# Performance work log

Measured on AMD Instinct MI355X. Metric: run time of the kernel, lower is better.

The kernel has to match this reference:

```python
import jax, jax.numpy as jnp
import numpy as np

B, IN, C, H, E = 8192, 768, 64, 64, 16  # batch, input_dim, n_concepts, hidden_dim, embedding_dim


def setup_inputs() -> dict:
    key = jax.random.key(0)
    ks = jax.random.split(key, 10)

    def w(k, shape, fan_in):
        return jax.random.normal(k, shape, jnp.float32) / np.float32(np.sqrt(fan_in))

    inp = {"x": jax.random.normal(ks[0], (B, IN), jnp.float32)}
    i = 1
    for pre, din, dout in (("pos", IN, E), ("neg", IN, E), ("cp", 2 * E, 1)):
        inp[pre + "_W1"] = w(ks[i], (C, din, H), din)
        inp[pre + "_b1"] = jnp.zeros((C, H), jnp.float32)
        inp[pre + "_W2"] = w(ks[i + 1], (C, H, H), H)
        inp[pre + "_b2"] = jnp.zeros((C, H), jnp.float32)
        inp[pre + "_W3"] = w(ks[i + 2], (C, H, dout), H)
        inp[pre + "_b3"] = jnp.zeros((C, dout), jnp.float32)
        i += 3
    return inp


def _bank(x, W1, b1, W2, b2, W3, b3):
    # x: [B, IN]; per-concept MLP batched over C via einsum -> [B, C, E]
    h = jax.nn.relu(jnp.einsum('bi,cih->bch', x, W1) + b1)
    h = jax.nn.relu(jnp.einsum('bch,cho->bco', h, W2) + b2)
    return jnp.einsum('bch,che->bce', h, W3) + b3


def reference(x, pos_W1, pos_b1, pos_W2, pos_b2, pos_W3, pos_b3,
              neg_W1, neg_b1, neg_W2, neg_b2, neg_W3, neg_b3,
              cp_W1, cp_b1, cp_W2, cp_b2, cp_W3, cp_b3):
    pos = _bank(x, pos_W1, pos_b1, pos_W2, pos_b2, pos_W3, pos_b3)  # [B,C,E]
    neg = _bank(x, neg_W1, neg_b1, neg_W2, neg_b2, neg_W3, neg_b3)  # [B,C,E]
    # torch cat([pos, neg], dim=1) on [B,E,C], then x[:,:,i] -> per-concept [B, 2E]
    xc = jnp.concatenate([pos, neg], axis=-1)  # [B,C,2E]
    h = jax.nn.relu(jnp.einsum('bci,cih->bch', xc, cp_W1) + cp_b1)
    h = jax.nn.relu(jnp.einsum('bch,cho->bco', h, cp_W2) + cp_b2)
    concepts = (jnp.einsum('bch,cho->bco', h, cp_W3) + cp_b3)[..., 0]  # [B,C]
    w = jnp.clip(concepts * 0.5 + 0.5, 0.0, 1.0)[:, :, None]  # gate in [0,1]
    emb = pos * w + neg * (1.0 - w)  # [B,C,E]
    # torch layout is [B,E,C] then .view(B,-1): transpose before flattening
    emb_flat = jnp.transpose(emb, (0, 2, 1)).reshape(x.shape[0], E * C)
    return emb_flat, concepts
```

## Files before the change

kernel.cpp:

```cpp
#include <hip/hip_runtime.h>
#include <hip/hip_bf16.h>


#define B_   8192
#define IN_  768
#define C_   64
#define H_   64
#define E_   16
#define BM_  128

typedef __bf16 bf16x8 __attribute__((ext_vector_type(8)));
typedef float  f32x4  __attribute__((ext_vector_type(4)));

__device__ __forceinline__ f32x4 mfma16(bf16x8 a, bf16x8 b, f32x4 c) {
  return __builtin_amdgcn_mfma_f32_16x16x32_bf16(a, b, c, 0, 0, 0);
}

__device__ __forceinline__ bf16x8 cvt8(float4 a, float4 b) {
  bf16x8 r;
  r[0] = (__bf16)a.x; r[1] = (__bf16)a.y; r[2] = (__bf16)a.z; r[3] = (__bf16)a.w;
  r[4] = (__bf16)b.x; r[5] = (__bf16)b.y; r[6] = (__bf16)b.z; r[7] = (__bf16)b.w;
  return r;
}

__device__ __forceinline__ void zero_acc(f32x4 (&acc)[2][4]) {
  const f32x4 z = {0.f, 0.f, 0.f, 0.f};
#pragma unroll
  for (int mt = 0; mt < 2; ++mt)
#pragma unroll
    for (int nt = 0; nt < 4; ++nt) acc[mt][nt] = z;
}

struct __align__(16) SmemT {
  __bf16 xs[BM_ * 72];
  __bf16 wt[64 * 72];
  __bf16 xcb[BM_ * 40];
  float  conc[BM_];
};
static_assert(sizeof(SmemT) <= 40960, "LDS overflow");

__device__ __forceinline__ void epi72(__bf16* __restrict__ hb, f32x4 (&acc)[2][4],
                                      const float* __restrict__ bias,
                                      int wave, int quad, int l16) {
#pragma unroll
  for (int nt = 0; nt < 4; ++nt) {
    const int col = nt * 16 + l16;
    const float bv = bias[col];
#pragma unroll
    for (int mt = 0; mt < 2; ++mt)
#pragma unroll
      for (int r = 0; r < 4; ++r) {
        int row = wave * 32 + mt * 16 + quad * 4 + r;
        hb[row * 72 + col] = (__bf16)fmaxf(acc[mt][nt][r] + bv, 0.f);
      }
  }
}

__device__ __forceinline__ void gemm64(const __bf16* __restrict__ hb,
                                       const __bf16* __restrict__ wt,
                                       f32x4 (&acc)[2][4], int wave, int quad, int l16) {
#pragma unroll
  for (int ks = 0; ks < 2; ++ks) {
    bf16x8 a[2], bb[4];
#pragma unroll
    for (int mt = 0; mt < 2; ++mt)
      a[mt] = *(const bf16x8*)(hb + (wave * 32 + mt * 16 + l16) * 72 + ks * 32 + quad * 8);
#pragma unroll
    for (int nt = 0; nt < 4; ++nt)
      bb[nt] = *(const bf16x8*)(wt + (nt * 16 + l16) * 72 + ks * 32 + quad * 8);
#pragma unroll
    for (int mt = 0; mt < 2; ++mt)
#pragma unroll
      for (int nt = 0; nt < 4; ++nt)
        acc[mt][nt] = mfma16(a[mt], bb[nt], acc[mt][nt]);
  }
}

__device__ __forceinline__ void stage_w64(const __bf16* __restrict__ Wt,
                                          __bf16* __restrict__ wt, int tid) {
#pragma unroll
  for (int it = 0; it < 2; ++it) {
    int q = tid + it * 256;
    int n = q >> 3, i = q & 7;
    *(uint4*)&wt[n * 72 + i * 8] = *(const uint4*)(Wt + n * 64 + i * 8);
  }
}

__device__ __forceinline__ void run_bank_t(SmemT& sm, const __bf16* __restrict__ x,
    const __bf16* __restrict__ W1t, const float* __restrict__ b1,
    const __bf16* __restrict__ W2t, const float* __restrict__ b2,
    const __bf16* __restrict__ W3t, const float* __restrict__ b3,
    int row0, int xc_off, int tid, int wave, int quad, int l16)
{
  __bf16* xs = sm.xs;
  __bf16* wt = sm.wt;
  __bf16* hb = sm.xs;

  f32x4 acc1[2][4]; zero_acc(acc1);
  const int sr = tid >> 3, si = tid & 7;
  const __bf16* xg = x + (size_t)row0 * IN_;
  for (int kt = 0; kt < IN_ / 64; ++kt) {
    const int ko = kt * 64;
    uint4 xv[4], wv[2];
#pragma unroll
    for (int it = 0; it < 4; ++it)
      xv[it] = *(const uint4*)(xg + (size_t)(sr + it * 32) * IN_ + ko + si * 8);
#pragma unroll
    for (int it = 0; it < 2; ++it)
      wv[it] = *(const uint4*)(W1t + (size_t)(sr + it * 32) * IN_ + ko + si * 8);
#pragma unroll
    for (int it = 0; it < 4; ++it)
      *(uint4*)&xs[(sr + it * 32) * 72 + si * 8] = xv[it];
#pragma unroll
    for (int it = 0; it < 2; ++it)
      *(uint4*)&wt[(sr + it * 32) * 72 + si * 8] = wv[it];
    __syncthreads();
#pragma unroll
    for (int ks = 0; ks < 2; ++ks) {
      bf16x8 a[2], bb[4];
#pragma unroll
      for (int mt = 0; mt < 2; ++mt)
        a[mt] = *(const bf16x8*)&xs[(wave * 32 + mt * 16 + l16) * 72 + ks * 32 + quad * 8];
#pragma unroll
      for (int nt = 0; nt < 4; ++nt)
        bb[nt] = *(const bf16x8*)&wt[(nt * 16 + l16) * 72 + ks * 32 + quad * 8];
#pragma unroll
      for (int mt = 0; mt < 2; ++mt)
#pragma unroll
        for (int nt = 0; nt < 4; ++nt)
          acc1[mt][nt] = mfma16(a[mt], bb[nt], acc1[mt][nt]);
    }
    __syncthreads();
  }
  epi72(hb, acc1, b1, wave, quad, l16);
  stage_w64(W2t, wt, tid);
  __syncthreads();

  f32x4 acc2[2][4]; zero_acc(acc2);
  gemm64(hb, wt, acc2, wave, quad, l16);
  __syncthreads();
  epi72(hb, acc2, b2, wave, quad, l16);
  if (tid < 128)
    *(uint4*)&wt[(tid >> 3) * 72 + (tid & 7) * 8] =
        *(const uint4*)(W3t + (tid >> 3) * 64 + (tid & 7) * 8);
  __syncthreads();

  f32x4 acc3[2];
  { const f32x4 z = {0.f, 0.f, 0.f, 0.f}; acc3[0] = z; acc3[1] = z; }
#pragma unroll
  for (int ks = 0; ks < 2; ++ks) {
    bf16x8 bb = *(const bf16x8*)&wt[l16 * 72 + ks * 32 + quad * 8];
#pragma unroll
    for (int mt = 0; mt < 2; ++mt) {
      bf16x8 a = *(const bf16x8*)&hb[(wave * 32 + mt * 16 + l16) * 72 + ks * 32 + quad * 8];
      acc3[mt] = mfma16(a, bb, acc3[mt]);
    }
  }
  {
    float bv = b3[l16];
#pragma unroll
    for (int mt = 0; mt < 2; ++mt)
#pragma unroll
      for (int r = 0; r < 4; ++r) {
        int row = wave * 32 + mt * 16 + quad * 4 + r;
        sm.xcb[row * 40 + xc_off + l16] = (__bf16)(acc3[mt][r] + bv);
      }
  }
  __syncthreads();
}

__global__ __launch_bounds__(256, 4) void cb_fused_t(
    const __bf16* __restrict__ x,
    const __bf16* __restrict__ pW1t, const float* __restrict__ pb1,
    const __bf16* __restrict__ pW2t, const float* __restrict__ pb2,
    const __bf16* __restrict__ pW3t, const float* __restrict__ pb3,
    const __bf16* __restrict__ nW1t, const float* __restrict__ nb1,
    const __bf16* __restrict__ nW2t, const float* __restrict__ nb2,
    const __bf16* __restrict__ nW3t, const float* __restrict__ nb3,
    const __bf16* __restrict__ cW1t, const float* __restrict__ cb1,
    const __bf16* __restrict__ cW2t, const float* __restrict__ cb2,
    const __bf16* __restrict__ cw3,  const float* __restrict__ cb3,
    float* __restrict__ out_emb, float* __restrict__ out_con)
{
  __shared__ SmemT sm;
  const int tid  = threadIdx.x;
  const int wave = tid >> 6, lane = tid & 63;
  const int quad = lane >> 4, l16 = lane & 15;
  const int row0 = blockIdx.x * BM_;
  const int c    = blockIdx.y;
  __bf16* hb = sm.xs;
  __bf16* wt = sm.wt;

  run_bank_t(sm, x, pW1t + (size_t)c * 64 * IN_, pb1 + c * 64,
             pW2t + (size_t)c * 64 * 64, pb2 + c * 64,
             pW3t + (size_t)c * 16 * 64, pb3 + c * 16,
             row0, 0, tid, wave, quad, l16);
  run_bank_t(sm, x, nW1t + (size_t)c * 64 * IN_, nb1 + c * 64,
             nW2t + (size_t)c * 64 * 64, nb2 + c * 64,
             nW3t + (size_t)c * 16 * 64, nb3 + c * 16,
             row0, 16, tid, wave, quad, l16);

  {
    int n = tid >> 2, i = tid & 3;
    *(uint4*)&wt[n * 72 + i * 8] = *(const uint4*)(cW1t + ((size_t)c * 64 + n) * 32 + i * 8);
  }
  __syncthreads();
  f32x4 acc1[2][4]; zero_acc(acc1);
  {
    bf16x8 a[2], bb[4];
#pragma unroll
    for (int mt = 0; mt < 2; ++mt)
      a[mt] = *(const bf16x8*)&sm.xcb[(wave * 32 + mt * 16 + l16) * 40 + quad * 8];
#pragma unroll
    for (int nt = 0; nt < 4; ++nt)
      bb[nt] = *(const bf16x8*)&wt[(nt * 16 + l16) * 72 + quad * 8];
#pragma unroll
    for (int mt = 0; mt < 2; ++mt)
#pragma unroll
      for (int nt = 0; nt < 4; ++nt)
        acc1[mt][nt] = mfma16(a[mt], bb[nt], acc1[mt][nt]);
  }
  __syncthreads();
  epi72(hb, acc1, cb1 + c * 64, wave, quad, l16);
  stage_w64(cW2t + (size_t)c * 64 * 64, wt, tid);
  __syncthreads();

  f32x4 acc2[2][4]; zero_acc(acc2);
  gemm64(hb, wt, acc2, wave, quad, l16);
  __syncthreads();
  epi72(hb, acc2, cb2 + c * 64, wave, quad, l16);
  if (tid < 8) *(uint4*)&wt[tid * 8] = *(const uint4*)(cw3 + (size_t)c * 64 + tid * 8);
  __syncthreads();

  f32x4 acc3[2];
  { const f32x4 z = {0.f, 0.f, 0.f, 0.f}; acc3[0] = z; acc3[1] = z; }
#pragma unroll
  for (int ks = 0; ks < 2; ++ks) {
    bf16x8 bb = {};
    if (l16 == 0) bb = *(const bf16x8*)&wt[ks * 32 + quad * 8];
#pragma unroll
    for (int mt = 0; mt < 2; ++mt) {
      bf16x8 a = *(const bf16x8*)&hb[(wave * 32 + mt * 16 + l16) * 72 + ks * 32 + quad * 8];
      acc3[mt] = mfma16(a, bb, acc3[mt]);
    }
  }
  if (l16 == 0) {
    float bv = cb3[c];
#pragma unroll
    for (int mt = 0; mt < 2; ++mt)
#pragma unroll
      for (int r = 0; r < 4; ++r)
        sm.conc[wave * 32 + mt * 16 + quad * 4 + r] = acc3[mt][r] + bv;
  }
  __syncthreads();

  for (int ii = tid; ii < BM_ * E_; ii += 256) {
    int row = ii >> 4, e = ii & 15;
    float cv = sm.conc[row];
    float w  = fminf(fmaxf(cv * 0.5f + 0.5f, 0.f), 1.f);
    float pv2 = (float)sm.xcb[row * 40 + e];
    float nv2 = (float)sm.xcb[row * 40 + 16 + e];
    out_emb[(size_t)(row0 + row) * (E_ * C_) + e * C_ + c] = pv2 * w + nv2 * (1.f - w);
  }
  if (tid < 128) out_con[(size_t)(row0 + tid) * C_ + c] = sm.conc[tid];
}

#define TSEG 5
#define PSEG 5
struct PrepArgs {
  const float* tsrc[TSEG];
  __bf16*      tdst[TSEG];
  int tstart[TSEG + 1];
  int ktiles[TSEG];
  const float* psrc[PSEG];
  __bf16*      pdst[PSEG];
  int pstart[PSEG + 1];
  int pchunks[PSEG];
  int kdiv8[PSEG];
  int N[PSEG];
  int tblocks;
};

__global__ __launch_bounds__(256) void prep_all(PrepArgs a) {
  const int tid = threadIdx.x;
  const int b = blockIdx.x;
  __shared__ __bf16 lt[64 * 72];
  if (b < a.tblocks) {
    int s = 0;
    while (s < TSEG - 1 && b >= a.tstart[s + 1]) ++s;
    const int idx = b - a.tstart[s];
    const int kt = idx % a.ktiles[s];
    const int c  = idx / a.ktiles[s];
    const int K  = a.ktiles[s] * 64;
    const float* src = a.tsrc[s] + (size_t)c * K * 64 + (size_t)kt * 64 * 64;
    __bf16*      dst = a.tdst[s] + (size_t)c * 64 * K + kt * 64;
    const int r = tid >> 4, c4 = (tid & 15) * 4;
#pragma unroll
    for (int it = 0; it < 4; ++it) {
      int k = r + it * 16;
      float4 v = *(const float4*)(src + (size_t)k * 64 + c4);
      lt[(c4 + 0) * 72 + k] = (__bf16)v.x;
      lt[(c4 + 1) * 72 + k] = (__bf16)v.y;
      lt[(c4 + 2) * 72 + k] = (__bf16)v.z;
      lt[(c4 + 3) * 72 + k] = (__bf16)v.w;
    }
    __syncthreads();
    const int n = tid >> 3, i = tid & 7;
#pragma unroll
    for (int it = 0; it < 2; ++it) {
      int nn = n + it * 32;
      *(uint4*)(dst + (size_t)nn * K + i * 8) = *(const uint4*)&lt[nn * 72 + i * 8];
    }
  } else {
    const int bb = b - a.tblocks;
    int s = 0;
    while (s < PSEG - 1 && bb >= a.pstart[s + 1]) ++s;
    const int lb  = bb - a.pstart[s];
    const int nch = a.pchunks[s];
    const int kc  = a.kdiv8[s];
    const int N   = a.N[s];
#pragma unroll
    for (int j = 0; j < 4; ++j) {
      const int li = (lb * 4 + j) * 256 + tid;
      if (li >= nch) break;
      if (N == 1) {
        const float4* src = (const float4*)a.psrc[s] + (size_t)li * 2;
        float4 v0 = src[0], v1 = src[1];
        *(uint4*)(a.pdst[s] + (size_t)li * 8) = __builtin_bit_cast(uint4, cvt8(v0, v1));
      } else {
        int rn = li / kc;
        int k0 = (li - rn * kc) * 8;
        int cc = rn / N;
        int n  = rn - cc * N;
        const float* src = a.psrc[s] + ((size_t)cc * kc * 8 + k0) * N + n;
        bf16x8 r;
#pragma unroll
        for (int jj = 0; jj < 8; ++jj) r[jj] = (__bf16)src[(size_t)jj * N];
        *(uint4*)(a.pdst[s] + (size_t)rn * kc * 8 + k0) = __builtin_bit_cast(uint4, r);
      }
    }
  }
}

extern "C" void kernel_launch(void* const* d_in, const int* in_sizes, int n_in,
                              void* d_out, int out_size, void* d_ws, size_t ws_size,
                              hipStream_t stream) {
  const float* xf   = (const float*)d_in[0];
  const float* pW1f = (const float*)d_in[1];
  const float* pb1f = (const float*)d_in[2];
  const float* pW2f = (const float*)d_in[3];
  const float* pb2f = (const float*)d_in[4];
  const float* pW3f = (const float*)d_in[5];
  const float* pb3f = (const float*)d_in[6];
  const float* nW1f = (const float*)d_in[7];
  const float* nb1f = (const float*)d_in[8];
  const float* nW2f = (const float*)d_in[9];
  const float* nb2f = (const float*)d_in[10];
  const float* nW3f = (const float*)d_in[11];
  const float* nb3f = (const float*)d_in[12];
  const float* cW1f = (const float*)d_in[13];
  const float* cb1f = (const float*)d_in[14];
  const float* cW2f = (const float*)d_in[15];
  const float* cb2f = (const float*)d_in[16];
  const float* cW3f = (const float*)d_in[17];
  const float* cb3f = (const float*)d_in[18];

  float* out_emb = (float*)d_out;
  float* out_con = out_emb + (size_t)B_ * E_ * C_;

  const int cx   = B_ * IN_;
  const int cW1c = C_ * IN_ * H_;
  const int cW2c = C_ * H_ * H_;
  const int cW3c = C_ * H_ * E_;
  const int ccW1 = C_ * 2 * E_ * H_;
  const int ccW3 = C_ * H_;

  __bf16* w = (__bf16*)d_ws;
  size_t o = 0;
  __bf16* xw   = w + o; o += cx;
  __bf16* pw1t = w + o; o += cW1c;
  __bf16* nw1t = w + o; o += cW1c;
  __bf16* pw2t = w + o; o += cW2c;
  __bf16* nw2t = w + o; o += cW2c;
  __bf16* cw2t = w + o; o += cW2c;
  __bf16* pw3t = w + o; o += cW3c;
  __bf16* nw3t = w + o; o += cW3c;
  __bf16* cw1t = w + o; o += ccW1;
  __bf16* cw3w = w + o; o += ccW3;

  PrepArgs a;
  int tb = 0, pb = 0;
  {
    const float* tsrc[TSEG] = {pW1f, nW1f, pW2f, nW2f, cW2f};
    __bf16*      tdst[TSEG] = {pw1t, nw1t, pw2t, nw2t, cw2t};
    const int    tk[TSEG]   = {12,   12,   1,    1,    1};
    for (int i = 0; i < TSEG; ++i) {
      a.tsrc[i] = tsrc[i]; a.tdst[i] = tdst[i]; a.ktiles[i] = tk[i];
      a.tstart[i] = tb;
      tb += tk[i] * C_;
    }
    a.tstart[TSEG] = tb;
    a.tblocks = tb;

    const float* psrc[PSEG] = {xf, cW3f, pW3f, nW3f, cW1f};
    __bf16*      pdst[PSEG] = {xw, cw3w, pw3t, nw3t, cw1t};
    const int    pKs[PSEG]  = {0,  0,    64,   64,   32};
    const int    pNs[PSEG]  = {1,  1,    16,   16,   64};
    const int    pels[PSEG] = {cx, ccW3, cW3c, cW3c, ccW1};
    for (int i = 0; i < PSEG; ++i) {
      a.psrc[i] = psrc[i]; a.pdst[i] = pdst[i];
      a.pchunks[i] = pels[i] / 8;
      a.kdiv8[i] = (pNs[i] == 1) ? (pels[i] / 8) : (pKs[i] / 8);
      a.N[i] = pNs[i];
      a.pstart[i] = pb;
      pb += (pels[i] / 8 + 1023) / 1024;
    }
    a.pstart[PSEG] = pb;
  }
  prep_all<<<tb + pb, 256, 0, stream>>>(a);

  dim3 grid(B_ / BM_, C_);
  cb_fused_t<<<grid, 256, 0, stream>>>(xw,
      pw1t, pb1f, pw2t, pb2f, pw3t, pb3f,
      nw1t, nb1f, nw2t, nb2f, nw3t, nb3f,
      cw1t, cb1f, cw2t, cb2f, cw3w, cb3f,
      out_emb, out_con);
}
```

Before: 335.3 us.

## Pre-swizzle x into MFMA fragment layout and tile W1 contiguously per k-tile

```diff
diff --git a/kernel.cpp b/kernel.cpp
--- a/kernel.cpp
+++ b/kernel.cpp
@@ -32,7 +32,7 @@
 }
 
 struct __align__(16) SmemT {
-  __bf16 xs[BM_ * 72];
+  __bf16 hb[BM_ * 72];
   __bf16 wt[64 * 72];
   __bf16 xcb[BM_ * 40];
   float  conc[BM_];
@@ -86,41 +86,25 @@
   }
 }
 
-__device__ __forceinline__ void run_bank_t(SmemT& sm, const __bf16* __restrict__ x,
-    const __bf16* __restrict__ W1t, const float* __restrict__ b1,
+__device__ __forceinline__ void run_bank_t(SmemT& sm, const __bf16* __restrict__ af,
+    const __bf16* __restrict__ W1k, const float* __restrict__ b1,
     const __bf16* __restrict__ W2t, const float* __restrict__ b2,
     const __bf16* __restrict__ W3t, const float* __restrict__ b3,
-    int row0, int xc_off, int tid, int wave, int quad, int l16)
+    int xc_off, int tid, int wave, int quad, int l16)
 {
-  __bf16* xs = sm.xs;
   __bf16* wt = sm.wt;
-  __bf16* hb = sm.xs;
+  __bf16* hb = sm.hb;
 
   f32x4 acc1[2][4]; zero_acc(acc1);
-  const int sr = tid >> 3, si = tid & 7;
-  const __bf16* xg = x + (size_t)row0 * IN_;
   for (int kt = 0; kt < IN_ / 64; ++kt) {
-    const int ko = kt * 64;
-    uint4 xv[4], wv[2];
-#pragma unroll
-    for (int it = 0; it < 4; ++it)
-      xv[it] = *(const uint4*)(xg + (size_t)(sr + it * 32) * IN_ + ko + si * 8);
-#pragma unroll
-    for (int it = 0; it < 2; ++it)
-      wv[it] = *(const uint4*)(W1t + (size_t)(sr + it * 32) * IN_ + ko + si * 8);
-#pragma unroll
-    for (int it = 0; it < 4; ++it)
-      *(uint4*)&xs[(sr + it * 32) * 72 + si * 8] = xv[it];
-#pragma unroll
-    for (int it = 0; it < 2; ++it)
-      *(uint4*)&wt[(sr + it * 32) * 72 + si * 8] = wv[it];
+    stage_w64(W1k + kt * 4096, wt, tid);
     __syncthreads();
 #pragma unroll
     for (int ks = 0; ks < 2; ++ks) {
       bf16x8 a[2], bb[4];
 #pragma unroll
       for (int mt = 0; mt < 2; ++mt)
-        a[mt] = *(const bf16x8*)&xs[(wave * 32 + mt * 16 + l16) * 72 + ks * 32 + quad * 8];
+        a[mt] = *(const bf16x8*)(af + ((kt * 2 + ks) * 2 + mt) * 512);
 #pragma unroll
       for (int nt = 0; nt < 4; ++nt)
         bb[nt] = *(const bf16x8*)&wt[(nt * 16 + l16) * 72 + ks * 32 + quad * 8];
@@ -170,7 +154,7 @@
 }
 
 __global__ __launch_bounds__(256, 4) void cb_fused_t(
-    const __bf16* __restrict__ x,
+    const __bf16* __restrict__ xfrag,
     const __bf16* __restrict__ pW1t, const float* __restrict__ pb1,
     const __bf16* __restrict__ pW2t, const float* __restrict__ pb2,
     const __bf16* __restrict__ pW3t, const float* __restrict__ pb3,
@@ -188,17 +172,19 @@
   const int quad = lane >> 4, l16 = lane & 15;
   const int row0 = blockIdx.x * BM_;
   const int c    = blockIdx.y;
-  __bf16* hb = sm.xs;
+  __bf16* hb = sm.hb;
   __bf16* wt = sm.wt;
 
-  run_bank_t(sm, x, pW1t + (size_t)c * 64 * IN_, pb1 + c * 64,
-             pW2t + (size_t)c * 64 * 64, pb2 + c * 64,
-             pW3t + (size_t)c * 16 * 64, pb3 + c * 16,
-             row0, 0, tid, wave, quad, l16);
-  run_bank_t(sm, x, nW1t + (size_t)c * 64 * IN_, nb1 + c * 64,
-             nW2t + (size_t)c * 64 * 64, nb2 + c * 64,
-             nW3t + (size_t)c * 16 * 64, nb3 + c * 16,
-             row0, 16, tid, wave, quad, l16);
+  const __bf16* af = xfrag + ((size_t)(blockIdx.x * 4 + wave)) * 24576 + (size_t)lane * 8;
+
+  run_bank_t(sm, af, pW1t + (size_t)c * 49152, pb1 + c * 64,
+             pW2t + (size_t)c * 4096, pb2 + c * 64,
+             pW3t + (size_t)c * 1024, pb3 + c * 16,
+             0, tid, wave, quad, l16);
+  run_bank_t(sm, af, nW1t + (size_t)c * 49152, nb1 + c * 64,
+             nW2t + (size_t)c * 4096, nb2 + c * 64,
+             nW3t + (size_t)c * 1024, nb3 + c * 16,
+             16, tid, wave, quad, l16);
 
   {
     int n = tid >> 2, i = tid & 3;
@@ -222,7 +208,7 @@
   }
   __syncthreads();
   epi72(hb, acc1, cb1 + c * 64, wave, quad, l16);
-  stage_w64(cW2t + (size_t)c * 64 * 64, wt, tid);
+  stage_w64(cW2t + (size_t)c * 4096, wt, tid);
   __syncthreads();
 
   f32x4 acc2[2][4]; zero_acc(acc2);
@@ -266,12 +252,14 @@
 }
 
 #define TSEG 5
-#define PSEG 5
+#define PSEG 4
 struct PrepArgs {
   const float* tsrc[TSEG];
   __bf16*      tdst[TSEG];
   int tstart[TSEG + 1];
   int ktiles[TSEG];
+  const float* xsrc;
+  __bf16*      xdst;
   const float* psrc[PSEG];
   __bf16*      pdst[PSEG];
   int pstart[PSEG + 1];
@@ -293,7 +281,7 @@
     const int c  = idx / a.ktiles[s];
     const int K  = a.ktiles[s] * 64;
     const float* src = a.tsrc[s] + (size_t)c * K * 64 + (size_t)kt * 64 * 64;
-    __bf16*      dst = a.tdst[s] + (size_t)c * 64 * K + kt * 64;
+    __bf16*      dst = a.tdst[s] + ((size_t)c * a.ktiles[s] + kt) * 4096;
     const int r = tid >> 4, c4 = (tid & 15) * 4;
 #pragma unroll
     for (int it = 0; it < 4; ++it) {
@@ -309,10 +297,22 @@
 #pragma unroll
     for (int it = 0; it < 2; ++it) {
       int nn = n + it * 32;
-      *(uint4*)(dst + (size_t)nn * K + i * 8) = *(const uint4*)&lt[nn * 72 + i * 8];
+      *(uint4*)(dst + nn * 64 + i * 8) = *(const uint4*)&lt[nn * 72 + i * 8];
+    }
+  } else if (b < a.tblocks + 256) {
+    const int rt  = b - a.tblocks;
+    const int l16 = tid & 15, quad = (tid >> 4) & 3, mt = (tid >> 6) & 1, ks = tid >> 7;
+    const float* srow = a.xsrc + ((size_t)rt * 32 + mt * 16 + l16) * IN_ + ks * 32 + quad * 8;
+    __bf16* drow = a.xdst + (size_t)rt * 24576 + ((size_t)ks * 2 + mt) * 512
+                 + (size_t)(quad * 16 + l16) * 8;
+#pragma unroll
+    for (int kt = 0; kt < 12; ++kt) {
+      const float* s = srow + kt * 64;
+      float4 v0 = *(const float4*)s, v1 = *(const float4*)(s + 4);
+      *(uint4*)(drow + (size_t)kt * 2048) = __builtin_bit_cast(uint4, cvt8(v0, v1));
     }
   } else {
-    const int bb = b - a.tblocks;
+    const int bb = b - a.tblocks - 256;
     int s = 0;
     while (s < PSEG - 1 && bb >= a.pstart[s + 1]) ++s;
     const int lb  = bb - a.pstart[s];
@@ -377,7 +377,7 @@
 
   __bf16* w = (__bf16*)d_ws;
   size_t o = 0;
-  __bf16* xw   = w + o; o += cx;
+  __bf16* xfr  = w + o; o += cx;
   __bf16* pw1t = w + o; o += cW1c;
   __bf16* nw1t = w + o; o += cW1c;
   __bf16* pw2t = w + o; o += cW2c;
@@ -402,11 +402,14 @@
     a.tstart[TSEG] = tb;
     a.tblocks = tb;
 
-    const float* psrc[PSEG] = {xf, cW3f, pW3f, nW3f, cW1f};
-    __bf16*      pdst[PSEG] = {xw, cw3w, pw3t, nw3t, cw1t};
-    const int    pKs[PSEG]  = {0,  0,    64,   64,   32};
-    const int    pNs[PSEG]  = {1,  1,    16,   16,   64};
-    const int    pels[PSEG] = {cx, ccW3, cW3c, cW3c, ccW1};
+    a.xsrc = xf;
+    a.xdst = xfr;
+
+    const float* psrc[PSEG] = {cW3f, pW3f, nW3f, cW1f};
+    __bf16*      pdst[PSEG] = {cw3w, pw3t, nw3t, cw1t};
+    const int    pKs[PSEG]  = {0,    64,   64,   32};
+    const int    pNs[PSEG]  = {1,    16,   16,   64};
+    const int    pels[PSEG] = {ccW3, cW3c, cW3c, ccW1};
     for (int i = 0; i < PSEG; ++i) {
       a.psrc[i] = psrc[i]; a.pdst[i] = pdst[i];
       a.pchunks[i] = pels[i] / 8;
@@ -417,10 +420,10 @@
     }
     a.pstart[PSEG] = pb;
   }
-  prep_all<<<tb + pb, 256, 0, stream>>>(a);
+  prep_all<<<tb + 256 + pb, 256, 0, stream>>>(a);
 
   dim3 grid(B_ / BM_, C_);
-  cb_fused_t<<<grid, 256, 0, stream>>>(xw,
+  cb_fused_t<<<grid, 256, 0, stream>>>(xfr,
       pw1t, pb1f, pw2t, pb2f, pw3t, pb3f,
       nw1t, nb1f, nw2t, nb2f, nw3t, nb3f,
       cw1t, cb1f, cw2t, cb2f, cw3w, cb3f,
```

Measured after the change: 367.2 us. 9.5% more time.
